# Performance work log

Hardware: AMD Instinct MI355X
Metric: run time of the kernel (lower is better)

## Reference

```python
import jax, jax.numpy as jnp
import numpy as np

EMB = 64
HEADS = 8
POOL = 2          # instruction_pool_size
TOK = 10          # tokens_per_instruction
CAP = 32          # max_capped_distances per axis -> tables have 2*CAP-1 rows


def setup_inputs() -> dict:
    key = jax.random.key(0)
    ks = jax.random.split(key, 8)
    scale = float(np.sqrt(6.0 / (TOK + EMB)))  # xavier-ish; exact init irrelevant for math
    return {
        "enc_cross": jax.random.uniform(ks[0], (POOL, TOK, EMB), jnp.float32, -scale, scale),
        "enc_h": jax.random.uniform(ks[1], (2 * CAP - 1, EMB), jnp.float32, -scale, scale),
        "enc_w": jax.random.uniform(ks[2], (2 * CAP - 1, EMB), jnp.float32, -scale, scale),
        "enc_d": jax.random.uniform(ks[3], (2 * CAP - 1, EMB), jnp.float32, -scale, scale),
        "w_cross": jax.random.uniform(ks[4], (HEADS, EMB), jnp.float32, -scale, scale),
        "w_h": jax.random.uniform(ks[5], (HEADS, EMB), jnp.float32, -scale, scale),
        "w_w": jax.random.uniform(ks[6], (HEADS, EMB), jnp.float32, -scale, scale),
        "w_d": jax.random.uniform(ks[7], (HEADS, EMB), jnp.float32, -scale, scale),
        "dim_q": 4116,
        "dim_k": 4116,
        "dim_i": 20,
        "dim_h": 16,
        "dim_w": 16,
        "dim_d": 16,
    }


def _rel_embed(n, table):
    # table: [2*cap-1, emb]; returns gathered relative-position embeddings [n, n, emb]
    cap = (table.shape[0] + 1) // 2
    r = jnp.arange(n)
    idx = jnp.clip(r[None, :] - r[:, None] + cap - 1, 0, 2 * cap - 2)
    return table[idx]


def reference(enc_cross, enc_h, enc_w, enc_d, w_cross, w_h, w_w, w_d,
              dim_q, dim_k, dim_i, dim_h, dim_w, dim_d):
    tok = enc_cross.shape[1]
    emb = enc_cross.shape[-1]
    heads = w_cross.shape[0]
    inv_temperature = emb ** -0.5

    # instruction -> content embeddings: first n_cat tables concatenated (label_indices=None path)
    n_cat = dim_i // tok
    cross_emb = enc_cross[:n_cat].reshape(1, n_cat * tok, emb)  # [1, dim_i, emb]

    row_e = _rel_embed(dim_h, enc_h)  # [h, h, emb]
    col_e = _rel_embed(dim_w, enc_w)  # [w, w, emb]
    dep_e = _rel_embed(dim_d, enc_d)  # [d, d, emb]

    cross_s = jnp.einsum('hc,bnc->bhn', w_cross, cross_emb)        # [1, heads, dim_i]
    row_s = jnp.einsum('hc,nmc->hnm', w_h, row_e)[None]            # [1, heads, h, h]
    col_s = jnp.einsum('hc,nmc->hnm', w_w, col_e)[None]            # [1, heads, w, w]
    dep_s = jnp.einsum('hc,nmc->hnm', w_d, dep_e)[None]            # [1, heads, d, d]

    # broadcast-add over (i j k | l m n) -> [1, heads, h, w, d, h, w, d]
    content = (row_s[:, :, :, None, None, :, None, None]
               + col_s[:, :, None, :, None, None, :, None]
               + dep_s[:, :, None, None, :, None, None, :]) / 3.0
    S = dim_h * dim_w * dim_d
    content = content.reshape(1, heads, S, S)

    scores = jnp.zeros((1, heads, dim_q, dim_k), jnp.float32)
    # instruction bias block: rows dim_i:, cols :dim_i
    scores = scores.at[:, :, dim_i:, :dim_i].set(
        jnp.broadcast_to(cross_s[:, :, None, :], (1, heads, dim_q - dim_i, dim_i)))
    # content bias block: rows dim_i:, cols dim_i:
    scores = scores.at[:, :, dim_i:, dim_i:].set(content)
    return scores * inv_temperature
```

## Files before the change

### kernel.cpp

```cpp
#include <hip/hip_runtime.h>


#define EMB 64
#define NHEADS 8
#define DIM_I 20
#define DIM_Q 4116
#define NCHUNK 1029

__global__ __launch_bounds__(256) void tables_kernel(
    const float* __restrict__ enc_cross,
    const float* __restrict__ enc_h,
    const float* __restrict__ enc_w,
    const float* __restrict__ enc_d,
    const float* __restrict__ w_cross,
    const float* __restrict__ w_h,
    const float* __restrict__ w_w,
    const float* __restrict__ w_d,
    float* __restrict__ tabs)
{
    const int tid = blockIdx.x * blockDim.x + threadIdx.x;
    const int total = NHEADS * DIM_I + 3 * NHEADS * 256;
    if (tid >= total) return;

    if (tid < NHEADS * DIM_I) {
        const int h = tid / DIM_I;
        const int n = tid % DIM_I;
        const float* wv = w_cross + h * EMB;
        const float* ev = enc_cross + n * EMB;
        float acc = 0.f;
        #pragma unroll
        for (int c = 0; c < EMB; ++c) acc += wv[c] * ev[c];
        tabs[tid] = acc * 0.125f;
    } else {
        const int u = tid - NHEADS * DIM_I;
        const int table = u >> 11;
        const int v = u & 2047;
        const int h = v >> 8;
        const int i = (v >> 4) & 15;
        const int l = v & 15;
        const int ridx = l - i + 31;
        const float* wv;
        const float* ev;
        if (table == 0)      { wv = w_h + h * EMB; ev = enc_h + ridx * EMB; }
        else if (table == 1) { wv = w_w + h * EMB; ev = enc_w + ridx * EMB; }
        else                 { wv = w_d + h * EMB; ev = enc_d + ridx * EMB; }
        float acc = 0.f;
        #pragma unroll
        for (int c = 0; c < EMB; ++c) acc += wv[c] * ev[c];
        tabs[tid] = acc * (0.125f / 3.0f);
    }
}

__global__ __launch_bounds__(256) void fill_kernel(
    const float* __restrict__ tabs, float* __restrict__ out)
{
    const int q = blockIdx.x;
    const int h = blockIdx.y;

    float4* rowp = (float4*)(out + ((size_t)h * DIM_Q + q) * DIM_Q);

    if (q < DIM_I) {
        const float4 z = make_float4(0.f, 0.f, 0.f, 0.f);
        for (int t = threadIdx.x; t < NCHUNK; t += 256) rowp[t] = z;
        return;
    }

    const float* cross  = tabs + h * DIM_I;
    const float* row_s  = tabs + 160 + h * 256;
    const float* col_s  = tabs + 160 + 2048 + h * 256;
    const float* dep_s  = tabs + 160 + 4096 + h * 256;

    const int r  = q - DIM_I;
    const int i  = r >> 8;
    const int j  = (r >> 4) & 15;
    const int kk = r & 15;
    const float* rs_row = row_s + i * 16;
    const float* cs_row = col_s + j * 16;
    const float* ds_row = dep_s + kk * 16;

    for (int t = threadIdx.x; t < NCHUNK; t += 256) {
        float4 v;
        if (t < 5) {
            const int k0 = 4 * t;
            v.x = cross[k0 + 0];
            v.y = cross[k0 + 1];
            v.z = cross[k0 + 2];
            v.w = cross[k0 + 3];
        } else {
            const int c0 = 4 * t - DIM_I;
            const int l  = c0 >> 8;
            const int m  = (c0 >> 4) & 15;
            const int n0 = c0 & 15;
            const float base = rs_row[l] + cs_row[m];
            v.x = base + ds_row[n0 + 0];
            v.y = base + ds_row[n0 + 1];
            v.z = base + ds_row[n0 + 2];
            v.w = base + ds_row[n0 + 3];
        }
        rowp[t] = v;
    }
}

extern "C" void kernel_launch(void* const* d_in, const int* in_sizes, int n_in,
                              void* d_out, int out_size, void* d_ws, size_t ws_size,
                              hipStream_t stream)
{
    const float* enc_cross = (const float*)d_in[0];
    const float* enc_h     = (const float*)d_in[1];
    const float* enc_w     = (const float*)d_in[2];
    const float* enc_d     = (const float*)d_in[3];
    const float* w_cross   = (const float*)d_in[4];
    const float* w_h       = (const float*)d_in[5];
    const float* w_w       = (const float*)d_in[6];
    const float* w_d       = (const float*)d_in[7];

    float* tabs = (float*)d_ws;

    tables_kernel<<<dim3(25), dim3(256), 0, stream>>>(
        enc_cross, enc_h, enc_w, enc_d, w_cross, w_h, w_w, w_d, tabs);

    fill_kernel<<<dim3(DIM_Q, NHEADS), dim3(256), 0, stream>>>(
        tabs, (float*)d_out);
}
```

Before: 569.1 us.

## Have each fill block write 16 output rows using shared-memory staged tables

The fill kernel now launches 2048 blocks that each cover 16 consecutive query rows sharing the same (h,i,j). The dep, row, col and cross tables are staged in shared memory, and the row+col sum is precomputed once per block, so each thread writes 16 rows per column chunk. The 20 zero rows per head are handled by 64 separate blocks. This cuts per-row index math and global table reads and gives more work per thread. The cost is fewer blocks, and the stores from each thread are strided across rows.

After: 593.1 us. 1.04x slower.

```diff
diff --git a/kernel.cpp b/kernel.cpp
--- a/kernel.cpp
+++ b/kernel.cpp
@@ -54,50 +54,64 @@
 __global__ __launch_bounds__(256) void fill_kernel(
     const float* __restrict__ tabs, float* __restrict__ out)
 {
-    const int q = blockIdx.x;
-    const int h = blockIdx.y;
+    const int tid = threadIdx.x;
+    const int bid = blockIdx.x;
 
-    float4* rowp = (float4*)(out + ((size_t)h * DIM_Q + q) * DIM_Q);
-
-    if (q < DIM_I) {
-        const float4 z = make_float4(0.f, 0.f, 0.f, 0.f);
-        for (int t = threadIdx.x; t < NCHUNK; t += 256) rowp[t] = z;
+    if (bid >= 2048) {
+        const int z = bid - 2048;
+        const int h = z >> 3;
+        const int part = z & 7;
+        float4* zp = (float4*)(out + (size_t)h * DIM_Q * DIM_Q);
+        const int ztotal = DIM_I * NCHUNK;
+        const int per = (ztotal + 7) / 8;
+        const int lo = part * per;
+        const int hi = min(ztotal, lo + per);
+        const float4 zv = make_float4(0.f, 0.f, 0.f, 0.f);
+        for (int v = lo + tid; v < hi; v += 256) zp[v] = zv;
         return;
     }
 
-    const float* cross  = tabs + h * DIM_I;
-    const float* row_s  = tabs + 160 + h * 256;
-    const float* col_s  = tabs + 160 + 2048 + h * 256;
-    const float* dep_s  = tabs + 160 + 4096 + h * 256;
+    const int h   = bid >> 8;
+    const int rem = bid & 255;
+    const int i   = rem >> 4;
+    const int j   = rem & 15;
 
-    const int r  = q - DIM_I;
-    const int i  = r >> 8;
-    const int j  = (r >> 4) & 15;
-    const int kk = r & 15;
-    const float* rs_row = row_s + i * 16;
-    const float* cs_row = col_s + j * 16;
-    const float* ds_row = dep_s + kk * 16;
+    __shared__ __align__(16) float s_dep[256];
+    __shared__ float s_cross[20];
+    __shared__ float s_rs[16];
+    __shared__ float s_cs[16];
+    __shared__ float s_blm[256];
 
-    for (int t = threadIdx.x; t < NCHUNK; t += 256) {
-        float4 v;
+    s_dep[tid] = tabs[160 + 4096 + h * 256 + tid];
+    if (tid < 20)                 s_cross[tid]    = tabs[h * DIM_I + tid];
+    if (tid >= 32 && tid < 48)    s_rs[tid - 32]  = tabs[160 + h * 256 + i * 16 + (tid - 32)];
+    if (tid >= 64 && tid < 80)    s_cs[tid - 64]  = tabs[160 + 2048 + h * 256 + j * 16 + (tid - 64)];
+    __syncthreads();
+    s_blm[tid] = s_rs[tid >> 4] + s_cs[tid & 15];
+    __syncthreads();
+
+    const int q0 = DIM_I + i * 256 + j * 16;
+    float4* p = (float4*)(out + ((size_t)h * DIM_Q + q0) * DIM_Q);
+
+    for (int t = tid; t < NCHUNK; t += 256) {
+        float4* pt = p + t;
         if (t < 5) {
             const int k0 = 4 * t;
-            v.x = cross[k0 + 0];
-            v.y = cross[k0 + 1];
-            v.z = cross[k0 + 2];
-            v.w = cross[k0 + 3];
+            const float4 v = make_float4(s_cross[k0], s_cross[k0 + 1],
+                                         s_cross[k0 + 2], s_cross[k0 + 3]);
+            #pragma unroll
+            for (int kk = 0; kk < 16; ++kk) pt[kk * NCHUNK] = v;
         } else {
             const int c0 = 4 * t - DIM_I;
-            const int l  = c0 >> 8;
-            const int m  = (c0 >> 4) & 15;
+            const float blm = s_blm[c0 >> 4];
             const int n0 = c0 & 15;
-            const float base = rs_row[l] + cs_row[m];
-            v.x = base + ds_row[n0 + 0];
-            v.y = base + ds_row[n0 + 1];
-            v.z = base + ds_row[n0 + 2];
-            v.w = base + ds_row[n0 + 3];
+            #pragma unroll
+            for (int kk = 0; kk < 16; ++kk) {
+                const float4 d = *(const float4*)&s_dep[kk * 16 + n0];
+                pt[kk * NCHUNK] = make_float4(blm + d.x, blm + d.y,
+                                              blm + d.z, blm + d.w);
+            }
         }
-        rowp[t] = v;
     }
 }
 
@@ -119,6 +133,6 @@
     tables_kernel<<<dim3(25), dim3(256), 0, stream>>>(
         enc_cross, enc_h, enc_w, enc_d, w_cross, w_h, w_w, w_d, tabs);
 
-    fill_kernel<<<dim3(DIM_Q, NHEADS), dim3(256), 0, stream>>>(
+    fill_kernel<<<dim3(2048 + 64), dim3(256), 0, stream>>>(
         tabs, (float*)d_out);
 }
```
